# Optimization experiments

Measured on AMD Instinct MI355X. Metric: run time of the kernel, lower is better.

The kernel has to match this reference:

```python
import jax, jax.numpy as jnp
from jax import lax
import numpy as np

DN = ('NCHW', 'OIHW', 'NCHW')


def _conv(x, w, b, stride):
    y = lax.conv_general_dilated(x, w, (stride, stride), 'VALID', dimension_numbers=DN)
    return jax.nn.relu(y + b[None, :, None, None])


def setup_inputs() -> dict:
    key = jax.random.key(0)
    ks = jax.random.split(key, 24)
    B = 1024
    s = 0.05
    inp = {
        'rgb_image': jax.random.normal(ks[0], (B, 15000), jnp.float32),
        'distance': jax.random.uniform(ks[1], (B,), jnp.float32),
        'speed': jax.random.uniform(ks[2], (B,), jnp.float32),
        # LaneFollower (PilotNet-style CNN) params
        'conv1_w': s * jax.random.normal(ks[3], (24, 1, 5, 5), jnp.float32),
        'conv1_b': jnp.zeros((24,), jnp.float32),
        'conv2_w': s * jax.random.normal(ks[4], (36, 24, 5, 5), jnp.float32),
        'conv2_b': jnp.zeros((36,), jnp.float32),
        'conv3_w': s * jax.random.normal(ks[5], (48, 36, 5, 5), jnp.float32),
        'conv3_b': jnp.zeros((48,), jnp.float32),
        'conv4_w': s * jax.random.normal(ks[6], (64, 48, 3, 3), jnp.float32),
        'conv4_b': jnp.zeros((64,), jnp.float32),
        'fc1_w': s * jax.random.normal(ks[7], (5120, 100), jnp.float32),
        'fc1_b': jnp.zeros((100,), jnp.float32),
        'fc2_w': s * jax.random.normal(ks[8], (100, 50), jnp.float32),
        'fc2_b': jnp.zeros((50,), jnp.float32),
        'fc3_w': s * jax.random.normal(ks[9], (50, 10), jnp.float32),
        'fc3_b': jnp.zeros((10,), jnp.float32),
        'fc4_w': s * jax.random.normal(ks[10], (10, 1), jnp.float32),
        'fc4_b': jnp.zeros((1,), jnp.float32),
        # AEBS MLP params: 3 -> 12 -> 24 -> 4
        'a1_w': s * jax.random.normal(ks[11], (3, 12), jnp.float32),
        'a1_b': jnp.zeros((12,), jnp.float32),
        'a2_w': s * jax.random.normal(ks[12], (12, 24), jnp.float32),
        'a2_b': jnp.zeros((24,), jnp.float32),
        'a3_w': s * jax.random.normal(ks[13], (24, 4), jnp.float32),
        'a3_b': jnp.zeros((4,), jnp.float32),
    }
    return inp


def reference(rgb_image, distance, speed,
              conv1_w, conv1_b, conv2_w, conv2_b, conv3_w, conv3_b, conv4_w, conv4_b,
              fc1_w, fc1_b, fc2_w, fc2_b, fc3_w, fc3_b, fc4_w, fc4_b,
              a1_w, a1_b, a2_w, a2_b, a3_w, a3_b):
    B = rgb_image.shape[0]
    # lane_follow_input[i, j] = 1 if flat[i + j*200] > 0 else 0  ==> transpose of (75,200) reshape
    x = jnp.where(rgb_image.reshape(B, 75, 200) > 0, 1.0, 0.0).transpose(0, 2, 1)
    x = x[:, None, :, :]  # [B,1,200,75]
    x = _conv(x, conv1_w, conv1_b, 2)  # [B,24,98,36]
    x = _conv(x, conv2_w, conv2_b, 2)  # [B,36,47,16]
    x = _conv(x, conv3_w, conv3_b, 2)  # [B,48,22,6]
    x = _conv(x, conv4_w, conv4_b, 1)  # [B,64,20,4]
    x = x.reshape(B, -1)  # [B,5120]
    x = jax.nn.relu(x @ fc1_w + fc1_b)
    x = jax.nn.relu(x @ fc2_w + fc2_b)
    x = jax.nn.relu(x @ fc3_w + fc3_b)
    steering = (x @ fc4_w + fc4_b)[:, 0]  # [B]
    steering = lax.stop_gradient(steering)  # torch.no_grad() on lane follower
    aebs_in = jnp.stack([steering, distance, speed], axis=-1)  # [B,3]
    h = jax.nn.relu(aebs_in @ a1_w + a1_b)
    h = jax.nn.relu(h @ a2_w + a2_b)
    brake_force = h @ a3_w + a3_b  # [B,4]
    return brake_force
```

## Files before the change

### kernel.cpp

```cpp
#include <hip/hip_runtime.h>

typedef _Float16 f16;
typedef _Float16 f16x4 __attribute__((ext_vector_type(4)));
typedef _Float16 f16x8 __attribute__((ext_vector_type(8)));
typedef float f32x4 __attribute__((ext_vector_type(4)));

__global__ __launch_bounds__(256) void repack_all_k(
    f16* __restrict__ w1c, f16* __restrict__ w2c, f16* __restrict__ w3m,
    f16* __restrict__ w4m, f16* __restrict__ wfc,
    const float* __restrict__ s1, const float* __restrict__ s2, const float* __restrict__ s3,
    const float* __restrict__ s4, const float* __restrict__ sf){
  const int tid0 = blockIdx.x*256 + threadIdx.x, stride = gridDim.x*256;
  for (int idx = tid0; idx < 1024; idx += stride){
    int i = idx & 7, l = (idx >> 3) & 63, mt = idx >> 9;
    int co = mt*16 + (l & 15);
    int jg = l >> 4;
    int kw = -1, kh = 0;
    if (jg < 2){ kw = jg*2 + (i >> 2); kh = i & 3; }
    else if (jg == 2){
      if (i < 4){ kw = 4; kh = i; }
      else if (i == 4){ kw = 0; kh = 4; }
      else if (i == 5){ kw = 1; kh = 4; }
    } else {
      if (i == 0){ kw = 4; kh = 4; }
      else if (i == 4){ kw = 2; kh = 4; }
      else if (i == 5){ kw = 3; kh = 4; }
    }
    f16 v = (f16)0.0f;
    if (co < 24 && kw >= 0) v = (f16)s1[co*25 + kh*5 + kw];
    w1c[idx] = v;
  }
  for (int idx = tid0; idx < 29184; idx += stride){
    int i = idx & 7, l = (idx >> 3) & 63, rest = idx >> 9;
    int mt = rest % 3, s = rest / 3;
    int co = mt*16 + (l & 15);
    int k = s*32 + (l >> 4)*8 + i;
    f16 v = (f16)0.0f;
    if (co < 36 && k < 600){
      int tap = k / 24, ci = k - tap*24;
      v = (f16)s2[(co*24 + ci)*25 + tap];
    }
    w2c[idx] = v;
  }
  for (int idx = tid0; idx < 44544; idx += stride){
    int i = idx & 7, l = (idx >> 3) & 63, rest = idx >> 9;
    int mt = rest % 3, s = rest / 3;
    int co = mt*16 + (l & 15);
    f16 v = (f16)0.0f;
    if (s < 25){
      int ci = (l >> 4)*8 + i;
      v = (f16)s3[(co*36 + ci)*25 + s];
    } else {
      int ke = (s - 25)*32 + (l >> 4)*8 + i;
      if (ke < 100){
        int p = ke >> 2, ci = 32 + (ke & 3);
        v = (f16)s3[(co*36 + ci)*25 + p];
      }
    }
    w3m[idx] = v;
  }
  for (int idx = tid0; idx < 28672; idx += stride){
    int i = idx & 7, l = (idx >> 3) & 63, rest = idx >> 9;
    int mt = rest & 3, s = rest >> 2;
    int co = mt*16 + (l & 15);
    int k = s*32 + (l >> 4)*8 + i;
    f16 v = (f16)0.0f;
    if (k < 432){
      int pos = k / 48, ci = k - pos*48;
      v = (f16)s4[(co*48 + ci)*9 + pos];
    }
    w4m[idx] = v;
  }
  for (int t = tid0; t < 71680; t += stride){
    int l = t & 63, rest = t >> 6;
    int nt = rest % 7, s = rest / 7;
    int j = nt*16 + (l & 15);
    int kb = s*32 + (l >> 4)*8;
    union { f16 h[8]; f16x8 v; } pk;
    #pragma unroll
    for (int i=0;i<8;++i){
      int k = kb + i;
      int row = (k & 63)*80 + (k >> 6);
      pk.h[i] = (j < 100) ? (f16)sf[(size_t)row*100 + j] : (f16)0.0f;
    }
    *(f16x8*)(wfc + (size_t)t*8) = pk.v;
  }
}

__global__ __launch_bounds__(256) void conv12_k(const float* __restrict__ rgb, const f16* __restrict__ w1m,
                                                const float* __restrict__ b1, const f16* __restrict__ w2c,
                                                const float* __restrict__ b2, f16* __restrict__ a2, int ib){
  __shared__ __align__(16) f16 xb[75*46 + 8];
  __shared__ __align__(16) f16 xt[2*19*18*24];
  const int tid = threadIdx.x, bx = blockIdx.x;
  const int i = bx / 6, t = bx - i*6;
  const int h0 = t*32, oh0 = t*8;
  const float* img = rgb + (size_t)(ib + i)*15000;
  for (int idx = tid; idx < 825; idx += 256){
    int w = idx / 11, h4 = idx - w*11;
    int hh = h4*4, h = h0 + hh;
    union { f16 hv[4]; uint u[2]; } pk;
    if (h < 200){
      float4 v = *(const float4*)(img + w*200 + h);
      pk.hv[0] = (v.x > 0.f) ? (f16)1.0f : (f16)0.0f;
      pk.hv[1] = (v.y > 0.f) ? (f16)1.0f : (f16)0.0f;
      pk.hv[2] = (v.z > 0.f) ? (f16)1.0f : (f16)0.0f;
      pk.hv[3] = (v.w > 0.f) ? (f16)1.0f : (f16)0.0f;
    } else {
      pk.u[0] = 0u; pk.u[1] = 0u;
    }
    *(uint*)(xb + w*46 + hh)     = pk.u[0];
    *(uint*)(xb + w*46 + hh + 2) = pk.u[1];
  }
  __syncthreads();
  const int wv = tid >> 6, lane = tid & 63;
  const int jgrp = lane >> 4, npx = lane & 15;
  {
    f16x8 a1f0 = *(const f16x8*)(w1m + (size_t)lane*8);
    f16x8 a1f1 = *(const f16x8*)(w1m + (size_t)(64 + lane)*8);
    const int tA = (jgrp < 2) ? jgrp*92 : ((jgrp == 2) ? 184 : 188);
    const int tC = (jgrp == 1) ? 138 : 46;
    const int tE = (jgrp == 2) ? 4  : ((jgrp == 3) ? 96  : 0);
    const int tF = (jgrp == 2) ? 50 : ((jgrp == 3) ? 142 : 0);
    f32x4 bv0, bv1;
    #pragma unroll
    for (int reg=0; reg<4; ++reg){
      int c0 = jgrp*4 + reg;
      int c1 = 16 + jgrp*4 + reg;
      bv0[reg] = b1[c0];
      bv1[reg] = (c1 < 24) ? b1[c1] : 0.f;
    }
    const int qn = (wv == 3) ? 10 : 11;
    union { uint d[4]; f16x8 v; } bqc, bqn;
    int pxt_c, rr_c, ow_c;
    {
      int pxt = wv*16 + npx;
      int px = (pxt > 683) ? 683 : pxt;
      int rr = px/36, ow = px - rr*36;
      const int base = 2*(ow*46 + rr);
      uint ra = *(const uint*)(xb + base + tA);
      uint rb = *(const uint*)(xb + base + tA + 2);
      uint rc = *(const uint*)(xb + base + tC);
      uint rd = *(const uint*)(xb + base + tC + 2);
      uint re = *(const unsigned short*)(xb + base + tE);
      uint rf = *(const unsigned short*)(xb + base + tF);
      bqc.d[0] = ra; bqc.d[1] = rb;
      bqc.d[2] = (jgrp < 2) ? rc : (re | (rf << 16));
      bqc.d[3] = rd;
      pxt_c = pxt; rr_c = rr; ow_c = ow;
    }
    for (int q=0; q<qn; ++q){
      int pxt_n = 0, rr_n = 0, ow_n = 0;
      if (q+1 < qn){
        int nt = wv + 4*(q+1);
        pxt_n = nt*16 + npx;
        int px = (pxt_n > 683) ? 683 : pxt_n;
        rr_n = px/36; ow_n = px - rr_n*36;
        const int base = 2*(ow_n*46 + rr_n);
        uint ra = *(const uint*)(xb + base + tA);
        uint rb = *(const uint*)(xb + base + tA + 2);
        uint rc = *(const uint*)(xb + base + tC);
        uint rd = *(const uint*)(xb + base + tC + 2);
        uint re = *(const unsigned short*)(xb + base + tE);
        uint rf = *(const unsigned short*)(xb + base + tF);
        bqn.d[0] = ra; bqn.d[1] = rb;
        bqn.d[2] = (jgrp < 2) ? rc : (re | (rf << 16));
        bqn.d[3] = rd;
      }
      f32x4 c0 = __builtin_amdgcn_mfma_f32_16x16x32_f16(a1f0, bqc.v, bv0, 0, 0, 0);
      f32x4 c1 = __builtin_amdgcn_mfma_f32_16x16x32_f16(a1f1, bqc.v, bv1, 0, 0, 0);
      if (pxt_c <= 683){
        f16* dst = xt + (((ow_c & 1)*19 + rr_c)*18 + (ow_c >> 1))*24;
        union { f16 h[4]; uint2 q2; } pk;
        #pragma unroll
        for (int reg=0; reg<4; ++reg){ float r = c0[reg]; if (r<0.f) r=0.f; pk.h[reg]=(f16)r; }
        *(uint2*)(dst + jgrp*4) = pk.q2;
        if (jgrp < 2){
          #pragma unroll
          for (int reg=0; reg<4; ++reg){ float r = c1[reg]; if (r<0.f) r=0.f; pk.h[reg]=(f16)r; }
          *(uint2*)(dst + 16 + jgrp*4) = pk.q2;
        }
      }
      if (q+1 < qn){ bqc.v = bqn.v; pxt_c = pxt_n; rr_c = rr_n; ow_c = ow_n; }
    }
  }
  __syncthreads();
  int baddr[19];
  #pragma unroll
  for (int s=0; s<19; ++s){
    int m = s*4 + jgrp;
    int tap = m / 3, r3 = m - tap*3;
    if (m >= 75){ tap = 24; r3 = 0; }
    int kh = tap / 5, kw = tap - kh*5;
    int par = kw & 1, kws = kw >> 1;
    baddr[s] = ((par*19 + kh)*18 + npx + kws)*24 + r3*8;
  }
  f32x4 acc2[3][2];
  #pragma unroll
  for (int mt=0; mt<3; ++mt){
    f32x4 bv;
    #pragma unroll
    for (int reg=0; reg<4; ++reg){
      int co = mt*16 + jgrp*4 + reg;
      bv[reg] = (co < 36) ? b2[co] : 0.0f;
    }
    acc2[mt][0] = bv; acc2[mt][1] = bv;
  }
  const f16* agl = w2c + (size_t)lane*8;
  const int rowo = 4*wv*432;
  f16x8 af0, af1, af2, bf0, bf1;
  {
    af0 = *(const f16x8*)(agl + 0*512);
    af1 = *(const f16x8*)(agl + 1*512);
    af2 = *(const f16x8*)(agl + 2*512);
    const f16* bb0 = xt + baddr[0] + rowo;
    bf0 = *(const f16x8*)(bb0);
    bf1 = *(const f16x8*)(bb0 + 2*432);
  }
  #pragma unroll
  for (int s=0; s<19; ++s){
    f16x8 naf0, naf1, naf2, nbf0, nbf1;
    if (s < 18){
      naf0 = *(const f16x8*)(agl + (size_t)((s+1)*3 + 0)*512);
      naf1 = *(const f16x8*)(agl + (size_t)((s+1)*3 + 1)*512);
      naf2 = *(const f16x8*)(agl + (size_t)((s+1)*3 + 2)*512);
      const f16* bb0 = xt + baddr[s+1] + rowo;
      nbf0 = *(const f16x8*)(bb0);
      nbf1 = *(const f16x8*)(bb0 + 2*432);
    }
    acc2[0][0] = __builtin_amdgcn_mfma_f32_16x16x32_f16(af0, bf0, acc2[0][0], 0, 0, 0);
    acc2[0][1] = __builtin_amdgcn_mfma_f32_16x16x32_f16(af0, bf1, acc2[0][1], 0, 0, 0);
    acc2[1][0] = __builtin_amdgcn_mfma_f32_16x16x32_f16(af1, bf0, acc2[1][0], 0, 0, 0);
    acc2[1][1] = __builtin_amdgcn_mfma_f32_16x16x32_f16(af1, bf1, acc2[1][1], 0, 0, 0);
    acc2[2][0] = __builtin_amdgcn_mfma_f32_16x16x32_f16(af2, bf0, acc2[2][0], 0, 0, 0);
    acc2[2][1] = __builtin_amdgcn_mfma_f32_16x16x32_f16(af2, bf1, acc2[2][1], 0, 0, 0);
    if (s < 18){
      af0 = naf0; af1 = naf1; af2 = naf2; bf0 = nbf0; bf1 = nbf1;
    }
  }
  #pragma unroll
  for (int u=0; u<2; ++u){
    const int oh = oh0 + 2*wv + u;
    if (oh >= 47) continue;
    #pragma unroll
    for (int mt=0; mt<3; ++mt){
      const int co0s = mt*16 + jgrp*4;
      if (co0s >= 36) continue;
      union { f16 h[4]; uint2 q; } pk;
      #pragma unroll
      for (int reg=0; reg<4; ++reg){
        float r = acc2[mt][u][reg]; if (r < 0.f) r = 0.f;
        pk.h[reg] = (f16)r;
      }
      *(uint2*)(a2 + (((size_t)i*47 + oh)*16 + npx)*36 + co0s) = pk.q;
    }
  }
}

__global__ __launch_bounds__(256) void conv34_k(const f16* __restrict__ a2, const f16* __restrict__ w3m,
                                                const float* __restrict__ b3, const f16* __restrict__ w4m,
                                                const float* __restrict__ b4, f16* __restrict__ a4){
  __shared__ __align__(16) f16 xt[27*680];
  __shared__ __align__(16) f16 a3t[12*6*56];
  const int tid = threadIdx.x, bx = blockIdx.x;
  const int i = bx >> 1, t = bx & 1;
  const int r0 = t*20, obase = t*10;
  {
    const uint2* s2 = (const uint2*)((const uint*)a2 + (size_t)i*13536);
    uint2* d = (uint2*)xt;
    for (int idx = tid; idx < 3888; idx += 256){
      int d2 = idx % 9, rc = idx / 9;
      int c = rc & 15, r = rc >> 4;
      int dwi = d2*2, jg = dwi >> 2, part = dwi & 3;
      d[(r*340 + jg*68 + c*4 + part) >> 1] = s2[((size_t)(r0 + r)*16 + c)*9 + d2];
    }
  }
  __syncthreads();
  const int wv = tid >> 6, lane = tid & 63;
  const int npx = lane & 15, jg = lane >> 4;
  {
    int baseq[2], ohl[2], owl[2];
    #pragma unroll
    for (int q=0;q<2;++q){
      int px = (wv*2+q)*16 + npx; if (px > 71) px = 71;
      ohl[q] = px/6; owl[q] = px - ohl[q]*6;
      baseq[q] = 2*ohl[q]*680 + jg*136 + 2*owl[q]*8;
    }
    f32x4 acc[3][2];
    #pragma unroll
    for (int mt=0;mt<3;++mt){
      f32x4 bv;
      #pragma unroll
      for (int reg=0;reg<4;++reg) bv[reg] = b3[mt*16 + jg*4 + reg];
      acc[mt][0]=bv; acc[mt][1]=bv;
    }
    const f16* agl = w3m + (size_t)lane*8;
    f16x8 caf0 = *(const f16x8*)(agl);
    f16x8 caf1 = *(const f16x8*)(agl + 512);
    f16x8 caf2 = *(const f16x8*)(agl + 1024);
    f16x8 cbf0 = *(const f16x8*)(xt + baseq[0]);
    f16x8 cbf1 = *(const f16x8*)(xt + baseq[1]);
    #pragma unroll
    for (int s=0; s<25; ++s){
      f16x8 naf0, naf1, naf2, nbf0, nbf1;
      if (s < 24){
        const int sn = s + 1;
        naf0 = *(const f16x8*)(agl + (size_t)(sn*3 + 0)*512);
        naf1 = *(const f16x8*)(agl + (size_t)(sn*3 + 1)*512);
        naf2 = *(const f16x8*)(agl + (size_t)(sn*3 + 2)*512);
        const int off = (sn/5)*680 + (sn%5)*8;
        nbf0 = *(const f16x8*)(xt + baseq[0] + off);
        nbf1 = *(const f16x8*)(xt + baseq[1] + off);
      }
      acc[0][0] = __builtin_amdgcn_mfma_f32_16x16x32_f16(caf0, cbf0, acc[0][0], 0, 0, 0);
      acc[0][1] = __builtin_amdgcn_mfma_f32_16x16x32_f16(caf0, cbf1, acc[0][1], 0, 0, 0);
      acc[1][0] = __builtin_amdgcn_mfma_f32_16x16x32_f16(caf1, cbf0, acc[1][0], 0, 0, 0);
      acc[1][1] = __builtin_amdgcn_mfma_f32_16x16x32_f16(caf1, cbf1, acc[1][1], 0, 0, 0);
      acc[2][0] = __builtin_amdgcn_mfma_f32_16x16x32_f16(caf2, cbf0, acc[2][0], 0, 0, 0);
      acc[2][1] = __builtin_amdgcn_mfma_f32_16x16x32_f16(caf2, cbf1, acc[2][1], 0, 0, 0);
      if (s < 24){ caf0=naf0; caf1=naf1; caf2=naf2; cbf0=nbf0; cbf1=nbf1; }
    }
    #pragma unroll
    for (int e=0;e<4;++e){
      const int s = 25 + e;
      f16x8 af[3];
      #pragma unroll
      for (int mt=0;mt<3;++mt)
        af[mt] = *(const f16x8*)(agl + (size_t)(s*3 + mt)*512);
      int p1 = e*8 + jg*2; int p2 = p1 + 1;
      if (p1 > 24) p1 = 24;
      if (p2 > 24) p2 = 24;
      const int kh1 = p1/5, kw1 = p1 - kh1*5;
      const int kh2 = p2/5, kw2 = p2 - kh2*5;
      #pragma unroll
      for (int q=0;q<2;++q){
        f16x4 lo = *(const f16x4*)(xt + (2*ohl[q]+kh1)*680 + 544 + (2*owl[q]+kw1)*8);
        f16x4 hi = *(const f16x4*)(xt + (2*ohl[q]+kh2)*680 + 544 + (2*owl[q]+kw2)*8);
        f16x8 bq = __builtin_shufflevector(lo, hi, 0,1,2,3,4,5,6,7);
        #pragma unroll
        for (int mt=0;mt<3;++mt)
          acc[mt][q] = __builtin_amdgcn_mfma_f32_16x16x32_f16(af[mt], bq, acc[mt][q], 0, 0, 0);
      }
    }
    #pragma unroll
    for (int q=0;q<2;++q){
      int px = (wv*2+q)*16 + npx;
      if (px >= 72) continue;
      #pragma unroll
      for (int mt=0;mt<3;++mt){
        union { f16 h[4]; uint2 q2; } pk;
        #pragma unroll
        for (int reg=0;reg<4;++reg){
          float r = acc[mt][q][reg]; if (r < 0.f) r = 0.f;
          pk.h[reg] = (f16)r;
        }
        *(uint2*)(a3t + px*56 + mt*16 + jg*4) = pk.q2;
      }
    }
  }
  __syncthreads();
  {
    f32x4 acc4[3];
    {
      f32x4 bv;
      #pragma unroll
      for (int reg=0;reg<4;++reg) bv[reg] = b4[wv*16 + jg*4 + reg];
      acc4[0]=bv; acc4[1]=bv; acc4[2]=bv;
    }
    int ohn[3], own[3];
    #pragma unroll
    for (int nt=0;nt<3;++nt){
      int px = nt*16 + npx; if (px > 39) px = 39;
      ohn[nt] = px >> 2; own[nt] = px & 3;
    }
    const f16* agl = w4m + (size_t)lane*8;
    f16x8 caf, cb0, cb1, cb2;
    {
      caf = *(const f16x8*)(agl + (size_t)wv*512);
      const int ci0 = jg*8;
      cb0 = *(const f16x8*)(a3t + (ohn[0]*6 + own[0])*56 + ci0);
      cb1 = *(const f16x8*)(a3t + (ohn[1]*6 + own[1])*56 + ci0);
      cb2 = *(const f16x8*)(a3t + (ohn[2]*6 + own[2])*56 + ci0);
    }
    #pragma unroll
    for (int s=0; s<14; ++s){
      f16x8 naf, nb0, nb1, nb2;
      if (s < 13){
        const int sn = s + 1;
        naf = *(const f16x8*)(agl + (size_t)(sn*4 + wv)*512);
        int k8 = sn*32 + jg*8;
        int pos, ci0;
        if (k8 >= 432){ pos = 8; ci0 = 40; }
        else { pos = k8 / 48; ci0 = k8 - pos*48; }
        const int kh = pos/3, kw = pos - kh*3;
        nb0 = *(const f16x8*)(a3t + ((ohn[0]+kh)*6 + own[0]+kw)*56 + ci0);
        nb1 = *(const f16x8*)(a3t + ((ohn[1]+kh)*6 + own[1]+kw)*56 + ci0);
        nb2 = *(const f16x8*)(a3t + ((ohn[2]+kh)*6 + own[2]+kw)*56 + ci0);
      }
      acc4[0] = __builtin_amdgcn_mfma_f32_16x16x32_f16(caf, cb0, acc4[0], 0, 0, 0);
      acc4[1] = __builtin_amdgcn_mfma_f32_16x16x32_f16(caf, cb1, acc4[1], 0, 0, 0);
      acc4[2] = __builtin_amdgcn_mfma_f32_16x16x32_f16(caf, cb2, acc4[2], 0, 0, 0);
      if (s < 13){ caf = naf; cb0 = nb0; cb1 = nb1; cb2 = nb2; }
    }
    #pragma unroll
    for (int nt=0;nt<3;++nt){
      int px = nt*16 + npx;
      if (px >= 40) continue;
      union { f16 h[4]; uint2 q2; } pk;
      #pragma unroll
      for (int reg=0;reg<4;++reg){
        float r = acc4[nt][reg]; if (r < 0.f) r = 0.f;
        pk.h[reg] = (f16)r;
      }
      *(uint2*)(a4 + ((size_t)i*80 + obase*4 + px)*64 + wv*16 + jg*4) = pk.q2;
    }
  }
}

__global__ __launch_bounds__(256) void fc1tail_k(const f16* __restrict__ a4, const f16* __restrict__ w1m,
    const float* __restrict__ fc1b, const float* __restrict__ dist, const float* __restrict__ speed,
    const float* __restrict__ fW2, const float* __restrict__ fb2,
    const float* __restrict__ fW3, const float* __restrict__ fb3,
    const float* __restrict__ fW4, const float* __restrict__ fb4,
    const float* __restrict__ aW1, const float* __restrict__ ab1,
    const float* __restrict__ aW2, const float* __restrict__ ab2,
    const float* __restrict__ aW3, const float* __restrict__ ab3,
    float* __restrict__ out, int ib, int n){
  __shared__ float red[4][64][28];
  __shared__ float x1s[8][100];
  __shared__ float h2s[8][50];
  __shared__ float h3s[8][10];
  __shared__ float stg[8];
  __shared__ float hb1[8][12];
  __shared__ float hb2[8][24];
  const int tid = threadIdx.x;
  const int wv = tid >> 6, lane = tid & 63;
  const int img0 = blockIdx.x*8;
  f32x4 acc[7];
  #pragma unroll
  for (int nt=0;nt<7;++nt) acc[nt] = (f32x4){0.f,0.f,0.f,0.f};
  int ia = img0 + (lane & 15);
  if (ia > n-1) ia = n-1;
  const f16* ap = a4 + (size_t)ia*5120 + (lane >> 4)*8;
  const f16* bp = w1m + (size_t)lane*8;
  const int s0 = wv*40;
  f16x8 cav = *(const f16x8*)(ap + s0*32);
  f16x8 cbv0 = *(const f16x8*)(bp + (size_t)(s0*7 + 0)*512);
  f16x8 cbv1 = *(const f16x8*)(bp + (size_t)(s0*7 + 1)*512);
  f16x8 cbv2 = *(const f16x8*)(bp + (size_t)(s0*7 + 2)*512);
  f16x8 cbv3 = *(const f16x8*)(bp + (size_t)(s0*7 + 3)*512);
  f16x8 cbv4 = *(const f16x8*)(bp + (size_t)(s0*7 + 4)*512);
  f16x8 cbv5 = *(const f16x8*)(bp + (size_t)(s0*7 + 5)*512);
  f16x8 cbv6 = *(const f16x8*)(bp + (size_t)(s0*7 + 6)*512);
  #pragma unroll 1
  for (int s = s0; s < s0 + 40; ++s){
    f16x8 nav, nbv0, nbv1, nbv2, nbv3, nbv4, nbv5, nbv6;
    const bool more = (s + 1 < s0 + 40);
    if (more){
      nav  = *(const f16x8*)(ap + (s+1)*32);
      nbv0 = *(const f16x8*)(bp + (size_t)((s+1)*7 + 0)*512);
      nbv1 = *(const f16x8*)(bp + (size_t)((s+1)*7 + 1)*512);
      nbv2 = *(const f16x8*)(bp + (size_t)((s+1)*7 + 2)*512);
      nbv3 = *(const f16x8*)(bp + (size_t)((s+1)*7 + 3)*512);
      nbv4 = *(const f16x8*)(bp + (size_t)((s+1)*7 + 4)*512);
      nbv5 = *(const f16x8*)(bp + (size_t)((s+1)*7 + 5)*512);
      nbv6 = *(const f16x8*)(bp + (size_t)((s+1)*7 + 6)*512);
    }
    acc[0] = __builtin_amdgcn_mfma_f32_16x16x32_f16(cav, cbv0, acc[0], 0, 0, 0);
    acc[1] = __builtin_amdgcn_mfma_f32_16x16x32_f16(cav, cbv1, acc[1], 0, 0, 0);
    acc[2] = __builtin_amdgcn_mfma_f32_16x16x32_f16(cav, cbv2, acc[2], 0, 0, 0);
    acc[3] = __builtin_amdgcn_mfma_f32_16x16x32_f16(cav, cbv3, acc[3], 0, 0, 0);
    acc[4] = __builtin_amdgcn_mfma_f32_16x16x32_f16(cav, cbv4, acc[4], 0, 0, 0);
    acc[5] = __builtin_amdgcn_mfma_f32_16x16x32_f16(cav, cbv5, acc[5], 0, 0, 0);
    acc[6] = __builtin_amdgcn_mfma_f32_16x16x32_f16(cav, cbv6, acc[6], 0, 0, 0);
    if (more){
      cav = nav;
      cbv0 = nbv0; cbv1 = nbv1; cbv2 = nbv2; cbv3 = nbv3;
      cbv4 = nbv4; cbv5 = nbv5; cbv6 = nbv6;
    }
  }
  {
    f32x4* accp = acc;
    #pragma unroll
    for (int nt=0;nt<7;++nt)
      #pragma unroll
      for (int reg=0;reg<4;++reg)
        red[wv][lane][nt*4+reg] = accp[nt][reg];
  }
  __syncthreads();
  for (int idx = tid; idx < 896; idx += 256){
    int imgl = idx / 112, j = idx - imgl*112;
    if (j >= 100) continue;
    int l = ((imgl >> 2) << 4) | (j & 15);
    int c = (j >> 4)*4 + (imgl & 3);
    float s = red[0][l][c] + red[1][l][c] + red[2][l][c] + red[3][l][c] + fc1b[j];
    x1s[imgl][j] = s > 0.f ? s : 0.f;
  }
  __syncthreads();
  const int g = tid >> 5, l32 = tid & 31;
  const int img = ib + img0 + g;
  for (int j = l32; j < 50; j += 32){
    float s = fb2[j];
    #pragma unroll 4
    for (int k = 0; k < 100; ++k) s = fmaf(x1s[g][k], fW2[k*50+j], s);
    h2s[g][j] = s > 0.f ? s : 0.f;
  }
  __syncthreads();
  if (l32 < 10){
    float s = fb3[l32];
    #pragma unroll
    for (int k = 0; k < 50; ++k) s = fmaf(h2s[g][k], fW3[k*10+l32], s);
    h3s[g][l32] = s > 0.f ? s : 0.f;
  }
  __syncthreads();
  if (l32 == 0){
    float s = fb4[0];
    #pragma unroll
    for (int k = 0; k < 10; ++k) s = fmaf(h3s[g][k], fW4[k], s);
    stg[g] = s;
  }
  __syncthreads();
  if (l32 < 12){
    float s0v = stg[g], dd = dist[img], sp = speed[img];
    float s = ab1[l32] + s0v*aW1[l32] + dd*aW1[12+l32] + sp*aW1[24+l32];
    hb1[g][l32] = s > 0.f ? s : 0.f;
  }
  __syncthreads();
  if (l32 < 24){
    float s = ab2[l32];
    #pragma unroll
    for (int k=0;k<12;++k) s = fmaf(hb1[g][k], aW2[k*24+l32], s);
    hb2[g][l32] = s > 0.f ? s : 0.f;
  }
  __syncthreads();
  if (l32 < 4){
    float s = ab3[l32];
    #pragma unroll
    for (int k=0;k<24;++k) s = fmaf(hb2[g][k], aW3[k*4+l32], s);
    out[(size_t)img*4 + l32] = s;
  }
}

extern "C" void kernel_launch(void* const* d_in, const int* in_sizes, int n_in,
                              void* d_out, int out_size, void* d_ws, size_t ws_size,
                              hipStream_t stream){
  const float* rgb   = (const float*)d_in[0];
  const float* dist  = (const float*)d_in[1];
  const float* speed = (const float*)d_in[2];
  const float* cw1 = (const float*)d_in[3];
  const float* cb1 = (const float*)d_in[4];
  const float* cw2 = (const float*)d_in[5];
  const float* cb2 = (const float*)d_in[6];
  const float* cw3 = (const float*)d_in[7];
  const float* cb3 = (const float*)d_in[8];
  const float* cw4 = (const float*)d_in[9];
  const float* cb4 = (const float*)d_in[10];
  const float* fW1 = (const float*)d_in[11];
  const float* fb1 = (const float*)d_in[12];
  const float* fW2 = (const float*)d_in[13];
  const float* fb2 = (const float*)d_in[14];
  const float* fW3 = (const float*)d_in[15];
  const float* fb3 = (const float*)d_in[16];
  const float* fW4 = (const float*)d_in[17];
  const float* fb4 = (const float*)d_in[18];
  const float* aW1 = (const float*)d_in[19];
  const float* ab1 = (const float*)d_in[20];
  const float* aW2 = (const float*)d_in[21];
  const float* ab2 = (const float*)d_in[22];
  const float* aW3 = (const float*)d_in[23];
  const float* ab3 = (const float*)d_in[24];
  float* out = (float*)d_out;
  const int B = in_sizes[0] / 15000;

  auto ALN = [](size_t x){ return (x + 255) & ~(size_t)255; };
  const size_t fixed = ALN(2048) + ALN(58368) + ALN(89088) + ALN(57344) + ALN(1146880);

  int nc = 1;
  while (nc < 32){
    size_t Bc = (size_t)(B / nc);
    size_t need = fixed + ALN(Bc*54144) + ALN(Bc*10240);
    if (need <= ws_size) break;
    nc *= 2;
  }
  const int Bc = B / nc;

  char* ws = (char*)d_ws;
  size_t o = 0;
  auto alloc = [&](size_t bytes)->char*{ char* p = ws + o; o += ALN(bytes); return p; };
  f16* w1c = (f16*)alloc(2048);
  f16* w2c = (f16*)alloc(58368);
  f16* w3m = (f16*)alloc(89088);
  f16* w4m = (f16*)alloc(57344);
  f16* w1m = (f16*)alloc(1146880);
  f16* a2  = (f16*)alloc((size_t)Bc*54144);
  f16* a4  = (f16*)alloc((size_t)Bc*10240);

  repack_all_k<<<dim3(280), dim3(256), 0, stream>>>(w1c, w2c, w3m, w4m, w1m,
                                                    cw1, cw2, cw3, cw4, fW1);

  for (int c = 0; c < nc; ++c){
    const int ib = c*Bc;
    conv12_k<<<dim3(Bc*6),  dim3(256), 0, stream>>>(rgb, w1c, cb1, w2c, cb2, a2, ib);
    conv34_k<<<dim3(Bc*2),  dim3(256), 0, stream>>>(a2, w3m, cb3, w4m, cb4, a4);
    fc1tail_k<<<dim3(Bc/8), dim3(256), 0, stream>>>(a4, w1m, fb1, dist, speed,
        fW2, fb2, fW3, fb3, fW4, fb4, aW1, ab1, aW2, ab2, aW3, ab3, out, ib, Bc);
  }
}
```

Before: 165.2 us.

## Swizzle block order across XCDs and halve images per fc1 block

Remaps block indices in all three main kernels so that consecutive logical blocks are spread in an XCD-aware interleaved order, meant to improve L2 locality and balance across the chiplets. The fc1tail kernel now handles 4 images per block instead of 8, doubling the grid and giving each wave one image in the tail MLP. The MFMA A operand now loads the 4 images replicated across the 16 rows. This wastes three quarters of the matrix-core work and reloads the fc1 weights twice as often, in exchange for more blocks and shorter per-block tails.

```diff
diff --git a/kernel.cpp b/kernel.cpp
--- a/kernel.cpp
+++ b/kernel.cpp
@@ -92,7 +92,9 @@
                                                 const float* __restrict__ b2, f16* __restrict__ a2, int ib){
   __shared__ __align__(16) f16 xb[75*46 + 8];
   __shared__ __align__(16) f16 xt[2*19*18*24];
-  const int tid = threadIdx.x, bx = blockIdx.x;
+  const int tid = threadIdx.x;
+  const int bxr = blockIdx.x;
+  const int bx = ((gridDim.x & 7) == 0) ? ((bxr & 7)*(gridDim.x >> 3) + (bxr >> 3)) : bxr;
   const int i = bx / 6, t = bx - i*6;
   const int h0 = t*32, oh0 = t*8;
   const float* img = rgb + (size_t)(ib + i)*15000;
@@ -262,7 +264,9 @@
                                                 const float* __restrict__ b4, f16* __restrict__ a4){
   __shared__ __align__(16) f16 xt[27*680];
   __shared__ __align__(16) f16 a3t[12*6*56];
-  const int tid = threadIdx.x, bx = blockIdx.x;
+  const int tid = threadIdx.x;
+  const int bxr = blockIdx.x;
+  const int bx = ((gridDim.x & 7) == 0) ? ((bxr & 7)*(gridDim.x >> 3) + (bxr >> 3)) : bxr;
   const int i = bx >> 1, t = bx & 1;
   const int r0 = t*20, obase = t*10;
   {
@@ -427,21 +431,21 @@
     const float* __restrict__ aW3, const float* __restrict__ ab3,
     float* __restrict__ out, int ib, int n){
   __shared__ float red[4][64][28];
-  __shared__ float x1s[8][100];
-  __shared__ float h2s[8][50];
-  __shared__ float h3s[8][10];
-  __shared__ float stg[8];
-  __shared__ float hb1[8][12];
-  __shared__ float hb2[8][24];
+  __shared__ float x1s[4][100];
+  __shared__ float h2s[4][50];
+  __shared__ float h3s[4][10];
+  __shared__ float stg[4];
+  __shared__ float hb1[4][12];
+  __shared__ float hb2[4][24];
   const int tid = threadIdx.x;
   const int wv = tid >> 6, lane = tid & 63;
-  const int img0 = blockIdx.x*8;
+  const int bxr = blockIdx.x;
+  const int bx = ((gridDim.x & 7) == 0) ? ((bxr & 7)*(gridDim.x >> 3) + (bxr >> 3)) : bxr;
+  const int img0 = bx*4;
   f32x4 acc[7];
   #pragma unroll
   for (int nt=0;nt<7;++nt) acc[nt] = (f32x4){0.f,0.f,0.f,0.f};
-  int ia = img0 + (lane & 15);
-  if (ia > n-1) ia = n-1;
-  const f16* ap = a4 + (size_t)ia*5120 + (lane >> 4)*8;
+  const f16* ap = a4 + (size_t)(img0 + ((lane & 15) & 3))*5120 + (lane >> 4)*8;
   const f16* bp = w1m + (size_t)lane*8;
   const int s0 = wv*40;
   f16x8 cav = *(const f16x8*)(ap + s0*32);
@@ -479,65 +483,62 @@
       cbv4 = nbv4; cbv5 = nbv5; cbv6 = nbv6;
     }
   }
-  {
-    f32x4* accp = acc;
-    #pragma unroll
-    for (int nt=0;nt<7;++nt)
-      #pragma unroll
-      for (int reg=0;reg<4;++reg)
-        red[wv][lane][nt*4+reg] = accp[nt][reg];
-  }
-  __syncthreads();
-  for (int idx = tid; idx < 896; idx += 256){
+  #pragma unroll
+  for (int nt=0;nt<7;++nt)
+    #pragma unroll
+    for (int reg=0;reg<4;++reg)
+      red[wv][lane][nt*4+reg] = acc[nt][reg];
+  __syncthreads();
+  for (int idx = tid; idx < 448; idx += 256){
     int imgl = idx / 112, j = idx - imgl*112;
     if (j >= 100) continue;
-    int l = ((imgl >> 2) << 4) | (j & 15);
-    int c = (j >> 4)*4 + (imgl & 3);
+    int l = j & 15;
+    int c = (j >> 4)*4 + imgl;
     float s = red[0][l][c] + red[1][l][c] + red[2][l][c] + red[3][l][c] + fc1b[j];
     x1s[imgl][j] = s > 0.f ? s : 0.f;
   }
   __syncthreads();
-  const int g = tid >> 5, l32 = tid & 31;
+  const int g = wv, l64 = lane;
   const int img = ib + img0 + g;
-  for (int j = l32; j < 50; j += 32){
-    float s = fb2[j];
+  if (l64 < 50){
+    float s = fb2[l64];
     #pragma unroll 4
-    for (int k = 0; k < 100; ++k) s = fmaf(x1s[g][k], fW2[k*50+j], s);
-    h2s[g][j] = s > 0.f ? s : 0.f;
-  }
-  __syncthreads();
-  if (l32 < 10){
-    float s = fb3[l32];
-    #pragma unroll
-    for (int k = 0; k < 50; ++k) s = fmaf(h2s[g][k], fW3[k*10+l32], s);
-    h3s[g][l32] = s > 0.f ? s : 0.f;
-  }
-  __syncthreads();
-  if (l32 == 0){
+    for (int k = 0; k < 100; ++k) s = fmaf(x1s[g][k], fW2[k*50+l64], s);
+    h2s[g][l64] = s > 0.f ? s : 0.f;
+  }
+  __syncthreads();
+  if (l64 < 10){
+    float s = fb3[l64];
+    #pragma unroll
+    for (int k = 0; k < 50; ++k) s = fmaf(h2s[g][k], fW3[k*10+l64], s);
+    h3s[g][l64] = s > 0.f ? s : 0.f;
+  }
+  __syncthreads();
+  if (l64 == 0){
     float s = fb4[0];
     #pragma unroll
     for (int k = 0; k < 10; ++k) s = fmaf(h3s[g][k], fW4[k], s);
     stg[g] = s;
   }
   __syncthreads();
-  if (l32 < 12){
+  if (l64 < 12){
     float s0v = stg[g], dd = dist[img], sp = speed[img];
-    float s = ab1[l32] + s0v*aW1[l32] + dd*aW1[12+l32] + sp*aW1[24+l32];
-    hb1[g][l32] = s > 0.f ? s : 0.f;
-  }
-  __syncthreads();
-  if (l32 < 24){
-    float s = ab2[l32];
-    #pragma unroll
-    for (int k=0;k<12;++k) s = fmaf(hb1[g][k], aW2[k*24+l32], s);
-    hb2[g][l32] = s > 0.f ? s : 0.f;
-  }
-  __syncthreads();
-  if (l32 < 4){
-    float s = ab3[l32];
-    #pragma unroll
-    for (int k=0;k<24;++k) s = fmaf(hb2[g][k], aW3[k*4+l32], s);
-    out[(size_t)img*4 + l32] = s;
+    float s = ab1[l64] + s0v*aW1[l64] + dd*aW1[12+l64] + sp*aW1[24+l64];
+    hb1[g][l64] = s > 0.f ? s : 0.f;
+  }
+  __syncthreads();
+  if (l64 < 24){
+    float s = ab2[l64];
+    #pragma unroll
+    for (int k=0;k<12;++k) s = fmaf(hb1[g][k], aW2[k*24+l64], s);
+    hb2[g][l64] = s > 0.f ? s : 0.f;
+  }
+  __syncthreads();
+  if (l64 < 4){
+    float s = ab3[l64];
+    #pragma unroll
+    for (int k=0;k<24;++k) s = fmaf(hb2[g][k], aW3[k*4+l64], s);
+    out[(size_t)img*4 + l64] = s;
   }
 }
 
@@ -602,7 +603,7 @@
     const int ib = c*Bc;
     conv12_k<<<dim3(Bc*6),  dim3(256), 0, stream>>>(rgb, w1c, cb1, w2c, cb2, a2, ib);
     conv34_k<<<dim3(Bc*2),  dim3(256), 0, stream>>>(a2, w3m, cb3, w4m, cb4, a4);
-    fc1tail_k<<<dim3(Bc/8), dim3(256), 0, stream>>>(a4, w1m, fb1, dist, speed,
+    fc1tail_k<<<dim3(Bc/4), dim3(256), 0, stream>>>(a4, w1m, fb1, dist, speed,
         fW2, fb2, fW3, fb3, fW4, fb4, aW1, ab1, aW2, ab2, aW3, ab3, out, ib, Bc);
   }
 }
```

Result: faster. 159.4 us (-3.5%).
